# Kernel tuning notes

Hardware: AMD Instinct MI355X
Metric: run time of the kernel (lower is better)

## Reference

```python
import jax, jax.numpy as jnp
import numpy as np

N = 100000
E = 1600000
D_IN, D_EMB, D_OUT = 16, 128, 2


def _mlp(x, W1, b1, W2, b2):
    return jax.nn.relu(x @ W1 + b1) @ W2 + b2


def _gcn(x, edge_index, edge_weight, W, b):
    # PyG GCNConv: x' = W x, symmetric norm with self-loops (weight 1), scatter-add, + bias
    n = x.shape[0]
    x = x @ W
    row, col = edge_index[0], edge_index[1]
    deg = jax.ops.segment_sum(edge_weight, col, num_segments=n) + 1.0  # +1 for self-loop
    dis = jax.lax.rsqrt(deg)
    norm = dis[row] * edge_weight * dis[col]                      # [E]
    agg = jax.ops.segment_sum(norm[:, None] * x[row], col, num_segments=n)
    agg = agg + (dis * dis)[:, None] * x                          # self-loop contribution
    return agg + b


def setup_inputs() -> dict:
    key = jax.random.key(0)
    ks = jax.random.split(key, 16)
    s_in = 1.0 / np.sqrt(D_IN)
    s_emb = 1.0 / np.sqrt(D_EMB)
    return {
        "x": jax.random.normal(ks[0], (N, D_IN), dtype=jnp.float32),
        "edge_index": jax.random.randint(ks[1], (2, E), 0, N, dtype=jnp.int64),
        "edge_weight": jax.random.uniform(ks[2], (E,), dtype=jnp.float32),
        # encoder MLP
        "enc_W1": jax.random.normal(ks[3], (D_IN, D_EMB), dtype=jnp.float32) * s_in,
        "enc_b1": jnp.zeros((D_EMB,), jnp.float32),
        "enc_W2": jax.random.normal(ks[4], (D_EMB, D_EMB), dtype=jnp.float32) * s_emb,
        "enc_b2": jnp.zeros((D_EMB,), jnp.float32),
        # conv1 / conv2
        "c1_W": jax.random.normal(ks[5], (D_EMB, D_EMB), dtype=jnp.float32) * s_emb,
        "c1_b": jnp.zeros((D_EMB,), jnp.float32),
        "c2_W": jax.random.normal(ks[6], (D_EMB, D_EMB), dtype=jnp.float32) * s_emb,
        "c2_b": jnp.zeros((D_EMB,), jnp.float32),
        # decoder MLP
        "dec_W1": jax.random.normal(ks[7], (D_EMB, D_EMB), dtype=jnp.float32) * s_emb,
        "dec_b1": jnp.zeros((D_EMB,), jnp.float32),
        "dec_W2": jax.random.normal(ks[8], (D_EMB, D_OUT), dtype=jnp.float32) * s_emb,
        "dec_b2": jnp.zeros((D_OUT,), jnp.float32),
    }


def reference(x, edge_index, edge_weight,
              enc_W1, enc_b1, enc_W2, enc_b2,
              c1_W, c1_b, c2_W, c2_b,
              dec_W1, dec_b1, dec_W2, dec_b2):
    h = _mlp(x, enc_W1, enc_b1, enc_W2, enc_b2)
    h = jax.nn.relu(_gcn(h, edge_index, edge_weight, c1_W, c1_b))
    h = jax.nn.relu(_gcn(h, edge_index, edge_weight, c2_W, c2_b))
    h = _mlp(h, dec_W1, dec_b1, dec_W2, dec_b2)
    return jax.nn.softmax(h, axis=1)
```

## Files before the change

kernel.cpp:

```cpp
#include <hip/hip_runtime.h>

#define N_NODES 100000
#define N_EDGES 1600000
#define NBKT 391
#define BKT_CAP 4608
#define PART_BLOCKS 782

typedef _Float16 half8 __attribute__((ext_vector_type(8)));
typedef float floatx4 __attribute__((ext_vector_type(4)));


__global__ __launch_bounds__(256) void k_part(const int* __restrict__ ei,
                                              const float* __restrict__ ew,
                                              unsigned* __restrict__ cursor,
                                              unsigned* __restrict__ partA,
                                              float* __restrict__ partB) {
    __shared__ unsigned hist[NBKT];
    __shared__ unsigned lrank[NBKT];
    __shared__ unsigned basebuf[NBKT];
    int tid = threadIdx.x;
    int e0 = blockIdx.x * 2048 + tid * 8;
    for (int i = tid; i < NBKT; i += 256) { hist[i] = 0; lrank[i] = 0; }
    __syncthreads();

    unsigned bk[8];
    bool full = (e0 + 8 <= N_EDGES);
    if (full) {
        #pragma unroll
        for (int v = 0; v < 2; v++) {
            int4 c = *(const int4*)(ei + N_EDGES + e0 + v * 4);
            bk[v * 4 + 0] = (unsigned)c.x >> 8;
            bk[v * 4 + 1] = (unsigned)c.y >> 8;
            bk[v * 4 + 2] = (unsigned)c.z >> 8;
            bk[v * 4 + 3] = (unsigned)c.w >> 8;
        }
        #pragma unroll
        for (int i = 0; i < 8; i++) atomicAdd(&hist[bk[i]], 1u);
    } else {
        for (int i = 0; i < 8; i++) {
            if (e0 + i < N_EDGES) {
                bk[i] = (unsigned)ei[N_EDGES + e0 + i] >> 8;
                atomicAdd(&hist[bk[i]], 1u);
            }
        }
    }
    __syncthreads();
    for (int b = tid; b < NBKT; b += 256) {
        unsigned h = hist[b];
        basebuf[b] = h ? atomicAdd(&cursor[b], h) : 0u;
    }
    __syncthreads();

    if (full) {
        #pragma unroll
        for (int v = 0; v < 2; v++) {
            int4 c = *(const int4*)(ei + N_EDGES + e0 + v * 4);
            int4 r = *(const int4*)(ei + e0 + v * 4);
            float4 w = *(const float4*)(ew + e0 + v * 4);
            int cols[4] = {c.x, c.y, c.z, c.w};
            int rows[4] = {r.x, r.y, r.z, r.w};
            float ws4[4] = {w.x, w.y, w.z, w.w};
            #pragma unroll
            for (int i = 0; i < 4; i++) {
                unsigned b = bk[v * 4 + i];
                unsigned rk = atomicAdd(&lrank[b], 1u);
                size_t idx = (size_t)b * BKT_CAP + basebuf[b] + rk;
                partA[idx] = (((unsigned)cols[i] & 255u) << 17) | (unsigned)rows[i];
                partB[idx] = ws4[i];
            }
        }
    } else {
        for (int i = 0; i < 8; i++) {
            if (e0 + i < N_EDGES) {
                int col = ei[N_EDGES + e0 + i];
                int row = ei[e0 + i];
                float wv = ew[e0 + i];
                unsigned b = bk[i];
                unsigned rk = atomicAdd(&lrank[b], 1u);
                size_t idx = (size_t)b * BKT_CAP + basebuf[b] + rk;
                partA[idx] = (((unsigned)col & 255u) << 17) | (unsigned)row;
                partB[idx] = wv;
            }
        }
    }
}

__global__ __launch_bounds__(256) void k_stats(const unsigned* __restrict__ cursor,
                                               const unsigned* __restrict__ partA,
                                               const float* __restrict__ partB,
                                               float* __restrict__ dis,
                                               int* __restrict__ offs,
                                               int* __restrict__ cnt) {
    __shared__ unsigned hist[256];
    __shared__ unsigned sc[256];
    __shared__ float dacc[256];
    int tid = threadIdx.x;
    int j = blockIdx.x;
    int count = (int)cursor[j];
    size_t p0 = (size_t)j * BKT_CAP;
    hist[tid] = 0;
    dacc[tid] = 0.f;
    __syncthreads();
    for (int i = tid; i < count; i += 256) {
        unsigned a = partA[p0 + i];
        float w = partB[p0 + i];
        unsigned cl = (a >> 17) & 255u;
        atomicAdd(&hist[cl], 1u);
        atomicAdd(&dacc[cl], w);
    }
    __syncthreads();
    unsigned myc = hist[tid];
    sc[tid] = myc;
    __syncthreads();
    #pragma unroll
    for (int d = 1; d < 256; d <<= 1) {
        unsigned t = (tid >= d) ? sc[tid - d] : 0u;
        __syncthreads();
        sc[tid] += t;
        __syncthreads();
    }
    int col = j * 256 + tid;
    if (col < N_NODES) {
        dis[col] = rsqrtf(dacc[tid] + 1.0f);
        cnt[col] = (int)myc;
        offs[col] = (int)(p0 + (sc[tid] - myc));
    }
}

__global__ __launch_bounds__(256) void k_scatter(const unsigned* __restrict__ cursor,
                                                 const unsigned* __restrict__ partA,
                                                 const float* __restrict__ partB,
                                                 const int* __restrict__ offs,
                                                 const float* __restrict__ dis,
                                                 unsigned* __restrict__ csr,
                                                 float* __restrict__ svec) {
    __shared__ unsigned cur[256];
    __shared__ float sacc[256];
    int tid = threadIdx.x;
    int j = blockIdx.x;
    int count = (int)cursor[j];
    size_t p0 = (size_t)j * BKT_CAP;
    int col = j * 256 + tid;
    cur[tid] = (col < N_NODES) ? (unsigned)(offs[col] - (int)p0) : 0u;
    sacc[tid] = 0.f;
    __syncthreads();
    for (int i = tid; i < count; i += 256) {
        unsigned a = partA[p0 + i];
        float wv = partB[p0 + i];
        unsigned cl = (a >> 17) & 255u;
        unsigned row = a & 0x1FFFFu;
        unsigned r = atomicAdd(&cur[cl], 1u);
        int colg = j * 256 + (int)cl;
        float w = dis[row] * wv * dis[colg];
        _Float16 hw = (_Float16)w;
        unsigned short hb;
        __builtin_memcpy(&hb, &hw, 2);
        csr[p0 + r] = ((unsigned)hb << 17) | row;
        atomicAdd(&sacc[cl], (float)hw);
    }
    __syncthreads();
    if (col < N_NODES) {
        float d = dis[col];
        svec[col] = sacc[tid] + d * d;
    }
}

__global__ __launch_bounds__(256) void prep_mm(const float* __restrict__ W2,
                                               const float* __restrict__ c1W,
                                               _Float16* __restrict__ Wt0) {
    __shared__ float sW[128 * 128];
    int t = threadIdx.x;
    for (int i = t; i < 4096; i += 256) ((float4*)sW)[i] = ((const float4*)c1W)[i];
    __syncthreads();
    int k = blockIdx.x * 2 + (t >> 7);
    int col = t & 127;
    float acc = 0.f;
    #pragma unroll 8
    for (int j = 0; j < 128; j++) acc = fmaf(W2[k * 128 + j], sW[j * 128 + col], acc);
    Wt0[col * 128 + k] = (_Float16)acc;
}

__global__ __launch_bounds__(128) void prep_bb(const float* __restrict__ b2,
                                               const float* __restrict__ c1W,
                                               float* __restrict__ bb) {
    int c = threadIdx.x;
    float acc = 0.f;
    for (int j = 0; j < 128; j++) acc = fmaf(b2[j], c1W[j * 128 + c], acc);
    bb[c] = acc;
}

__global__ __launch_bounds__(256) void prep_tr(const float* __restrict__ Wa,
                                               const float* __restrict__ Wb,
                                               _Float16* __restrict__ Wt) {
    int m = blockIdx.x >> 4;
    const float* W = (m == 0) ? Wa : Wb;
    _Float16* o = Wt + (m + 1) * 16384;
    int base = (blockIdx.x & 15) * 1024 + threadIdx.x * 4;
    int col = base >> 7;
    int k0 = base & 127;
    #pragma unroll
    for (int i = 0; i < 4; i++) o[base + i] = (_Float16)W[(k0 + i) * 128 + col];
}


__global__ __launch_bounds__(256) void enc1_kernel(const float* __restrict__ x,
                                                   const float* __restrict__ W1,
                                                   const float* __restrict__ b1,
                                                   _Float16* __restrict__ out) {
    __shared__ float sX[256 * 17];
    __shared__ float sW[2048];
    __shared__ float sb[128];
    int t = threadIdx.x;
    int base = blockIdx.x * 256;
    for (int i = t; i < 512; i += 256) ((float4*)sW)[i] = ((const float4*)W1)[i];
    if (t < 128) sb[t] = b1[t];
    #pragma unroll
    for (int i = 0; i < 4; i++) {
        int f = i * 1024 + t * 4;
        int row = f >> 4, k = f & 15;
        float4 v = make_float4(0.f, 0.f, 0.f, 0.f);
        if (base + row < N_NODES) v = *(const float4*)(x + (size_t)(base + row) * 16 + k);
        *(float4*)(sX + row * 17 + k) = v;
    }
    __syncthreads();
    int row = base + t;
    if (row >= N_NODES) return;
    float xr[16];
    #pragma unroll
    for (int k = 0; k < 16; k++) xr[k] = sX[t * 17 + k];
    #pragma unroll 4
    for (int cb = 0; cb < 16; cb++) {
        float acc[8];
        #pragma unroll
        for (int jj = 0; jj < 8; jj++) acc[jj] = sb[cb * 8 + jj];
        #pragma unroll
        for (int k = 0; k < 16; k++) {
            float xv = xr[k];
            #pragma unroll
            for (int jj = 0; jj < 8; jj++) acc[jj] = fmaf(xv, sW[k * 128 + cb * 8 + jj], acc[jj]);
        }
        half8 h;
        #pragma unroll
        for (int jj = 0; jj < 8; jj++) h[jj] = (_Float16)fmaxf(acc[jj], 0.f);
        *(half8*)(out + (size_t)row * 128 + cb * 8) = h;
    }
}


template <bool BIAS, bool RELU, bool DEC, bool SB>
__global__ __launch_bounds__(256, 2) void gemm_mfma(const _Float16* __restrict__ A,
                                                    const _Float16* __restrict__ Wt,
                                                    const float* __restrict__ bias,
                                                    _Float16* __restrict__ C,
                                                    const float* __restrict__ W2,
                                                    const float* __restrict__ b2,
                                                    float* __restrict__ sm_out,
                                                    const float* __restrict__ svec,
                                                    const float* __restrict__ bbv) {
    __shared__ _Float16 sA[2 * 64 * 128];
    __shared__ _Float16 sE[DEC ? 64 : 64 * 128];
    __shared__ float sW2[DEC ? 256 : 1];
    int t = threadIdx.x;
    int lane = t & 63;
    int w = t >> 6;
    int l15 = lane & 15;
    int l4 = lane >> 4;
    int stride = gridDim.x;

    half8 bfrag[8][4];
    #pragma unroll
    for (int n = 0; n < 8; n++)
        #pragma unroll
        for (int kk = 0; kk < 4; kk++)
            bfrag[n][kk] = *(const half8*)(Wt + (n * 16 + l15) * 128 + kk * 32 + l4 * 8);

    float bcol[8];
    if constexpr (BIAS) {
        #pragma unroll
        for (int n = 0; n < 8; n++) bcol[n] = bias[n * 16 + l15];
    }
    float bbcol[8];
    if constexpr (SB) {
        #pragma unroll
        for (int n = 0; n < 8; n++) bbcol[n] = bbv[n * 16 + l15];
    }
    float b20 = 0.f, b21 = 0.f;
    if constexpr (DEC) {
        if (t < 256) sW2[t] = W2[t];
        b20 = b2[0]; b21 = b2[1];
    }

    auto STAGE = [&](int buf, int tile) {
        const _Float16* Ag = A + (size_t)tile * 64 * 128;
        #pragma unroll
        for (int i = 0; i < 4; i++) {
            int c = i * 256 + t;
            int row = c >> 4;
            int g = (c & 15) ^ (row & 7);
            const _Float16* src = Ag + row * 128 + g * 8;
            __builtin_amdgcn_global_load_lds(
                (const __attribute__((address_space(1))) void*)src,
                (__attribute__((address_space(3))) void*)(sA + buf * 8192 + (size_t)(i * 256 + w * 64) * 8),
                16, 0, 0);
        }
    };

    const int NT = (N_NODES + 63) / 64;
    int cur = 0;
    STAGE(0, blockIdx.x);

    for (int tile = blockIdx.x; tile < NT; tile += stride) {
        int nx = tile + stride;
        if (nx < NT) {
            STAGE(cur ^ 1, nx);
            asm volatile("s_waitcnt vmcnt(4)" ::: "memory");
        } else {
            asm volatile("s_waitcnt vmcnt(0)" ::: "memory");
        }
        __builtin_amdgcn_s_barrier();
        asm volatile("" ::: "memory");

        const _Float16* sAc = sA + cur * 8192;

        floatx4 acc[8];
        #pragma unroll
        for (int n = 0; n < 8; n++) acc[n] = (floatx4)(0.f);

        #pragma unroll
        for (int kk = 0; kk < 4; kk++) {
            int rloc = w * 16 + l15;
            int cl = kk * 4 + l4;
            int s = cl ^ (rloc & 7);
            half8 af = *(const half8*)(sAc + rloc * 128 + s * 8);
            #pragma unroll
            for (int n = 0; n < 8; n++)
                acc[n] = __builtin_amdgcn_mfma_f32_16x16x32_f16(af, bfrag[n][kk], acc[n], 0, 0, 0);
        }

        size_t base_row = (size_t)tile * 64;
        float s4[4];
        if constexpr (SB) {
            #pragma unroll
            for (int r = 0; r < 4; r++) {
                int rr = (int)base_row + w * 16 + l4 * 4 + r;
                s4[r] = (rr < N_NODES) ? svec[rr] : 0.f;
            }
        }
        if constexpr (DEC) {
            #pragma unroll
            for (int r = 0; r < 4; r++) {
                float p0 = 0.f, p1 = 0.f;
                #pragma unroll
                for (int n = 0; n < 8; n++) {
                    float v = acc[n][r];
                    if constexpr (BIAS) v += bcol[n];
                    if constexpr (RELU) v = fmaxf(v, 0.f);
                    int ch = n * 16 + l15;
                    p0 = fmaf(v, sW2[ch * 2 + 0], p0);
                    p1 = fmaf(v, sW2[ch * 2 + 1], p1);
                }
                #pragma unroll
                for (int m = 1; m < 16; m <<= 1) {
                    p0 += __shfl_xor(p0, m, 64);
                    p1 += __shfl_xor(p1, m, 64);
                }
                size_t grow = base_row + w * 16 + l4 * 4 + r;
                if (l15 == 0 && grow < N_NODES) {
                    float z0 = p0 + b20, z1 = p1 + b21;
                    float mx = fmaxf(z0, z1);
                    float e0 = expf(z0 - mx), e1 = expf(z1 - mx);
                    float si = 1.f / (e0 + e1);
                    *(float2*)(sm_out + grow * 2) = make_float2(e0 * si, e1 * si);
                }
            }
            __builtin_amdgcn_s_barrier();
            asm volatile("" ::: "memory");
        } else {
            #pragma unroll
            for (int n = 0; n < 8; n++) {
                #pragma unroll
                for (int r = 0; r < 4; r++) {
                    float v = acc[n][r];
                    if constexpr (SB) v += s4[r] * bbcol[n];
                    if constexpr (BIAS) v += bcol[n];
                    if constexpr (RELU) v = fmaxf(v, 0.f);
                    int row = w * 16 + l4 * 4 + r;
                    sE[row * 128 + n * 16 + l15] = (_Float16)v;
                }
            }
            __builtin_amdgcn_s_barrier();
            asm volatile("" ::: "memory");
            #pragma unroll
            for (int i = 0; i < 4; i++) {
                int c = i * 256 + t;
                int row = c >> 4;
                if (base_row + row < N_NODES) {
                    *(float4*)((char*)C + (base_row + row) * 256 + (c & 15) * 16) =
                        *(const float4*)((const char*)sE + (size_t)c * 16);
                }
            }
        }
        cur ^= 1;
    }
}


__device__ __forceinline__ float wdec(unsigned u) {
    unsigned short b = (unsigned short)(u >> 17);
    _Float16 h;
    __builtin_memcpy(&h, &b, 2);
    return (float)h;
}

__global__ __launch_bounds__(256) void agg_kernel(const _Float16* __restrict__ m,
                                                  const int* __restrict__ offs,
                                                  const int* __restrict__ cnt,
                                                  const unsigned* __restrict__ csr,
                                                  const float* __restrict__ dis,
                                                  _Float16* __restrict__ out) {
    int wave = threadIdx.x >> 6;
    int lane = threadIdx.x & 63;
    int g = lane >> 4;
    int q = lane & 15;
    int j = blockIdx.x * 4 + wave;
    if (j >= N_NODES) return;
    int s = offs[j];
    int num = cnt[j];
    unsigned qoff = (unsigned)(q * 8);

    float acc[8];
    if (g == 0) {
        float d = dis[j];
        float dd = d * d;
        half8 mv = *(const half8*)(m + (((unsigned)j << 7) | qoff));
        #pragma unroll
        for (int i = 0; i < 8; i++) acc[i] = dd * (float)mv[i];
    } else {
        #pragma unroll
        for (int i = 0; i < 8; i++) acc[i] = 0.f;
    }

    for (int e = 0; e < num; e += 16) {
        float wv[4];
        unsigned off[4];
        #pragma unroll
        for (int k = 0; k < 4; k++) {
            int idx = e + k * 4 + g;
            int idc = (idx < num) ? idx : (num - 1);
            unsigned uu = csr[s + idc];
            wv[k] = (idx < num) ? wdec(uu) : 0.f;
            off[k] = ((uu & 0x1FFFFu) << 7) | qoff;
        }
        half8 r0 = *(const half8*)(m + off[0]);
        half8 r1 = *(const half8*)(m + off[1]);
        half8 r2 = *(const half8*)(m + off[2]);
        half8 r3 = *(const half8*)(m + off[3]);
        #pragma unroll
        for (int i = 0; i < 8; i++) acc[i] = fmaf(wv[0], (float)r0[i], acc[i]);
        #pragma unroll
        for (int i = 0; i < 8; i++) acc[i] = fmaf(wv[1], (float)r1[i], acc[i]);
        #pragma unroll
        for (int i = 0; i < 8; i++) acc[i] = fmaf(wv[2], (float)r2[i], acc[i]);
        #pragma unroll
        for (int i = 0; i < 8; i++) acc[i] = fmaf(wv[3], (float)r3[i], acc[i]);
    }

    #pragma unroll
    for (int i = 0; i < 8; i++) {
        acc[i] += __shfl_xor(acc[i], 16, 64);
        acc[i] += __shfl_xor(acc[i], 32, 64);
    }

    if (g == 0) {
        half8 o;
        #pragma unroll
        for (int i = 0; i < 8; i++) o[i] = (_Float16)acc[i];
        *(half8*)(out + (((unsigned)j << 7) | qoff)) = o;
    }
}


extern "C" void kernel_launch(void* const* d_in, const int* in_sizes, int n_in,
                              void* d_out, int out_size, void* d_ws, size_t ws_size,
                              hipStream_t stream) {
    const float* x      = (const float*)d_in[0];
    const int*   ei     = (const int*)d_in[1];
    const float* ew     = (const float*)d_in[2];
    const float* enc_W1 = (const float*)d_in[3];
    const float* enc_b1 = (const float*)d_in[4];
    const float* enc_W2 = (const float*)d_in[5];
    const float* enc_b2 = (const float*)d_in[6];
    const float* c1_W   = (const float*)d_in[7];
    const float* c1_b   = (const float*)d_in[8];
    const float* c2_W   = (const float*)d_in[9];
    const float* c2_b   = (const float*)d_in[10];
    const float* dec_W1 = (const float*)d_in[11];
    const float* dec_b1 = (const float*)d_in[12];
    const float* dec_W2 = (const float*)d_in[13];
    const float* dec_b2 = (const float*)d_in[14];
    float* out = (float*)d_out;

    char* ws = (char*)d_ws;
    unsigned* partA = (unsigned*)(ws);
    float*    partB = (float*)(ws + 7206912);
    _Float16* B1 = (_Float16*)(ws);
    _Float16* B2 = (_Float16*)(ws + 25600000);
    _Float16* Wt = (_Float16*)(ws + 51200000);
    unsigned* cursor = (unsigned*)(ws + 51331072);
    float* dis     = (float*)(ws + 51333120);
    int*   offs    = (int*)  (ws + 51733120);
    int*   cnt     = (int*)  (ws + 52133120);
    unsigned* csr  = (unsigned*)(ws + 52533120);
    float* svec    = (float*)(ws + 59740032);
    float* bb      = (float*)(ws + 60140032);

    hipMemsetAsync(cursor, 0, 2048, stream);

    k_part<<<PART_BLOCKS, 256, 0, stream>>>(ei, ew, cursor, partA, partB);
    k_stats<<<NBKT, 256, 0, stream>>>(cursor, partA, partB, dis, offs, cnt);
    k_scatter<<<NBKT, 256, 0, stream>>>(cursor, partA, partB, offs, dis, csr, svec);

    prep_mm<<<64, 256, 0, stream>>>(enc_W2, c1_W, Wt);
    prep_bb<<<1, 128, 0, stream>>>(enc_b2, c1_W, bb);
    prep_tr<<<32, 256, 0, stream>>>(c2_W, dec_W1, Wt);
    enc1_kernel<<<(N_NODES + 255) / 256, 256, 0, stream>>>(x, enc_W1, enc_b1, B1);

    agg_kernel<<<N_NODES / 4, 256, 0, stream>>>(B1, offs, cnt, csr, dis, B2);
    gemm_mfma<true, true, false, true><<<781, 256, 0, stream>>>(
        B2, Wt + 0 * 16384, c1_b, B1, nullptr, nullptr, nullptr, svec, bb);
    agg_kernel<<<N_NODES / 4, 256, 0, stream>>>(B1, offs, cnt, csr, dis, B2);
    gemm_mfma<true, true, false, false><<<781, 256, 0, stream>>>(
        B2, Wt + 1 * 16384, c2_b, B1, nullptr, nullptr, nullptr, nullptr, nullptr);
    gemm_mfma<true, true, true, false><<<1563, 256, 0, stream>>>(
        B1, Wt + 2 * 16384, dec_b1, nullptr, dec_W2, dec_b2, out, nullptr, nullptr);
}
```

Measured before the change: 392.2 us.

## Replace atomic edge bucketing with deterministic count/scan/place CSR build

Rebuilds the CSR preprocessing as a multi-kernel pipeline: per-chunk bucket histograms, a per-bucket prefix scan for bases, wave-ballot ranking to place packed 64-bit edge records, a per-bucket LDS sort by column, and a per-node final pass computing normalized fp16 weights. This removes global atomics and the memset, and makes edge order deterministic. The cost is more launches and serial per-thread loops in the degree and final passes. The GEMM kernels also switch to a fixed persistent grid of 522 blocks and add LDS waitcnts before barriers.

```diff
diff --git a/kernel.cpp b/kernel.cpp
--- a/kernel.cpp
+++ b/kernel.cpp
@@ -4,166 +4,214 @@
 #define N_EDGES 1600000
 #define NBKT 391
 #define BKT_CAP 4608
-#define PART_BLOCKS 782
+#define NCHUNK 782
+#define CHUNK_E 2048
+#define GEMM_GRID 522
 
 typedef _Float16 half8 __attribute__((ext_vector_type(8)));
 typedef float floatx4 __attribute__((ext_vector_type(4)));
 
 
-__global__ __launch_bounds__(256) void k_part(const int* __restrict__ ei,
-                                              const float* __restrict__ ew,
-                                              unsigned* __restrict__ cursor,
-                                              unsigned* __restrict__ partA,
-                                              float* __restrict__ partB) {
+__global__ __launch_bounds__(256) void k_count(const int* __restrict__ ei,
+                                               unsigned* __restrict__ Mcnt) {
     __shared__ unsigned hist[NBKT];
-    __shared__ unsigned lrank[NBKT];
-    __shared__ unsigned basebuf[NBKT];
     int tid = threadIdx.x;
-    int e0 = blockIdx.x * 2048 + tid * 8;
-    for (int i = tid; i < NBKT; i += 256) { hist[i] = 0; lrank[i] = 0; }
-    __syncthreads();
-
-    unsigned bk[8];
-    bool full = (e0 + 8 <= N_EDGES);
-    if (full) {
+    int e0 = blockIdx.x * CHUNK_E + tid * 8;
+    for (int i = tid; i < NBKT; i += 256) hist[i] = 0;
+    __syncthreads();
+    if (e0 + 8 <= N_EDGES) {
         #pragma unroll
         for (int v = 0; v < 2; v++) {
             int4 c = *(const int4*)(ei + N_EDGES + e0 + v * 4);
-            bk[v * 4 + 0] = (unsigned)c.x >> 8;
-            bk[v * 4 + 1] = (unsigned)c.y >> 8;
-            bk[v * 4 + 2] = (unsigned)c.z >> 8;
-            bk[v * 4 + 3] = (unsigned)c.w >> 8;
-        }
-        #pragma unroll
-        for (int i = 0; i < 8; i++) atomicAdd(&hist[bk[i]], 1u);
+            atomicAdd(&hist[(unsigned)c.x >> 8], 1u);
+            atomicAdd(&hist[(unsigned)c.y >> 8], 1u);
+            atomicAdd(&hist[(unsigned)c.z >> 8], 1u);
+            atomicAdd(&hist[(unsigned)c.w >> 8], 1u);
+        }
     } else {
         for (int i = 0; i < 8; i++) {
-            if (e0 + i < N_EDGES) {
-                bk[i] = (unsigned)ei[N_EDGES + e0 + i] >> 8;
-                atomicAdd(&hist[bk[i]], 1u);
-            }
-        }
-    }
-    __syncthreads();
-    for (int b = tid; b < NBKT; b += 256) {
-        unsigned h = hist[b];
-        basebuf[b] = h ? atomicAdd(&cursor[b], h) : 0u;
-    }
-    __syncthreads();
-
-    if (full) {
-        #pragma unroll
-        for (int v = 0; v < 2; v++) {
-            int4 c = *(const int4*)(ei + N_EDGES + e0 + v * 4);
-            int4 r = *(const int4*)(ei + e0 + v * 4);
-            float4 w = *(const float4*)(ew + e0 + v * 4);
-            int cols[4] = {c.x, c.y, c.z, c.w};
-            int rows[4] = {r.x, r.y, r.z, r.w};
-            float ws4[4] = {w.x, w.y, w.z, w.w};
-            #pragma unroll
-            for (int i = 0; i < 4; i++) {
-                unsigned b = bk[v * 4 + i];
-                unsigned rk = atomicAdd(&lrank[b], 1u);
-                size_t idx = (size_t)b * BKT_CAP + basebuf[b] + rk;
-                partA[idx] = (((unsigned)cols[i] & 255u) << 17) | (unsigned)rows[i];
-                partB[idx] = ws4[i];
-            }
-        }
-    } else {
-        for (int i = 0; i < 8; i++) {
-            if (e0 + i < N_EDGES) {
-                int col = ei[N_EDGES + e0 + i];
-                int row = ei[e0 + i];
-                float wv = ew[e0 + i];
-                unsigned b = bk[i];
-                unsigned rk = atomicAdd(&lrank[b], 1u);
-                size_t idx = (size_t)b * BKT_CAP + basebuf[b] + rk;
-                partA[idx] = (((unsigned)col & 255u) << 17) | (unsigned)row;
-                partB[idx] = wv;
-            }
-        }
-    }
-}
-
-__global__ __launch_bounds__(256) void k_stats(const unsigned* __restrict__ cursor,
-                                               const unsigned* __restrict__ partA,
-                                               const float* __restrict__ partB,
-                                               float* __restrict__ dis,
-                                               int* __restrict__ offs,
-                                               int* __restrict__ cnt) {
+            if (e0 + i < N_EDGES)
+                atomicAdd(&hist[(unsigned)ei[N_EDGES + e0 + i] >> 8], 1u);
+        }
+    }
+    __syncthreads();
+    for (int i = tid; i < NBKT; i += 256) Mcnt[i * NCHUNK + blockIdx.x] = hist[i];
+}
+
+__global__ __launch_bounds__(256) void k_base(const unsigned* __restrict__ Mcnt,
+                                              unsigned* __restrict__ Mbase,
+                                              unsigned* __restrict__ btot) {
+    __shared__ unsigned s[256];
+    int t = threadIdx.x;
+    int j = blockIdx.x;
+    const unsigned* src = Mcnt + (size_t)j * NCHUNK;
+    unsigned* dst = Mbase + (size_t)j * NCHUNK;
+    unsigned carry = 0;
+    for (int seg = 0; seg < NCHUNK; seg += 256) {
+        int idx = seg + t;
+        unsigned v = (idx < NCHUNK) ? src[idx] : 0u;
+        s[t] = v;
+        __syncthreads();
+        for (int d = 1; d < 256; d <<= 1) {
+            unsigned u = (t >= d) ? s[t - d] : 0u;
+            __syncthreads();
+            s[t] += u;
+            __syncthreads();
+        }
+        if (idx < NCHUNK) dst[idx] = s[t] - v + carry;
+        carry += s[255];
+        __syncthreads();
+    }
+    if (t == 0) btot[j] = carry;
+}
+
+
+__global__ __launch_bounds__(64) void k_place(const int* __restrict__ ei,
+                                              const float* __restrict__ ew,
+                                              const unsigned* __restrict__ Mbase,
+                                              unsigned long long* __restrict__ part) {
+    __shared__ unsigned lrank[NBKT];
+    int lane = threadIdx.x;
+    int p = blockIdx.x;
+    int e0 = p * CHUNK_E;
+    int nloc = N_EDGES - e0; if (nloc > CHUNK_E) nloc = CHUNK_E;
+    for (int i = lane; i < NBKT; i += 64) lrank[i] = Mbase[i * NCHUNK + p];
+    __syncthreads();
+    for (int it = 0; it < CHUNK_E; it += 64) {
+        if (it >= nloc) break;
+        int li = it + lane;
+        bool valid = li < nloc;
+        unsigned col = 0, row = 0; float wv = 0.f;
+        if (valid) {
+            col = (unsigned)ei[N_EDGES + e0 + li];
+            row = (unsigned)ei[e0 + li];
+            wv = ew[e0 + li];
+        }
+        unsigned bk = col >> 8;
+        unsigned long long m = __ballot(valid ? 1 : 0);
+        #pragma unroll
+        for (int b = 0; b < 9; b++) {
+            unsigned long long bal = __ballot((bk >> b) & 1u);
+            m &= ((bk >> b) & 1u) ? bal : ~bal;
+        }
+        unsigned rank = (unsigned)__popcll(m & ((1ull << lane) - 1ull));
+        unsigned cntk = (unsigned)__popcll(m);
+        unsigned base = lrank[bk];
+        if (valid) {
+            unsigned u; __builtin_memcpy(&u, &wv, 4);
+            unsigned long long pay = ((unsigned long long)u << 32)
+                                   | (((unsigned long long)(col & 255u)) << 17)
+                                   | (unsigned long long)row;
+            part[(size_t)bk * BKT_CAP + base + rank] = pay;
+        }
+        bool leader = valid && (lane == (__ffsll((long long)m) - 1));
+        if (leader) lrank[bk] = base + cntk;
+        __syncthreads();
+    }
+}
+
+__global__ __launch_bounds__(64) void k_colsort(const unsigned* __restrict__ btot,
+                                                const unsigned long long* __restrict__ part,
+                                                unsigned long long* __restrict__ sorted,
+                                                float* __restrict__ dis,
+                                                int* __restrict__ offs,
+                                                int* __restrict__ cnt) {
+    __shared__ unsigned long long sh[BKT_CAP];
     __shared__ unsigned hist[256];
-    __shared__ unsigned sc[256];
-    __shared__ float dacc[256];
-    int tid = threadIdx.x;
+    __shared__ unsigned cbase[256];
+    __shared__ unsigned cur[256];
+    int lane = threadIdx.x;
     int j = blockIdx.x;
-    int count = (int)cursor[j];
+    int count = (int)btot[j];
     size_t p0 = (size_t)j * BKT_CAP;
-    hist[tid] = 0;
-    dacc[tid] = 0.f;
-    __syncthreads();
-    for (int i = tid; i < count; i += 256) {
-        unsigned a = partA[p0 + i];
-        float w = partB[p0 + i];
-        unsigned cl = (a >> 17) & 255u;
+    for (int i = lane; i < 256; i += 64) hist[i] = 0;
+    __syncthreads();
+    for (int i = lane; i < count; i += 64) {
+        unsigned cl = (unsigned)(part[p0 + i] >> 17) & 255u;
         atomicAdd(&hist[cl], 1u);
-        atomicAdd(&dacc[cl], w);
-    }
-    __syncthreads();
-    unsigned myc = hist[tid];
-    sc[tid] = myc;
-    __syncthreads();
-    #pragma unroll
-    for (int d = 1; d < 256; d <<= 1) {
-        unsigned t = (tid >= d) ? sc[tid - d] : 0u;
+    }
+    __syncthreads();
+    unsigned h0 = hist[lane * 4], h1 = hist[lane * 4 + 1];
+    unsigned h2 = hist[lane * 4 + 2], h3 = hist[lane * 4 + 3];
+    unsigned lsum = h0 + h1 + h2 + h3;
+    unsigned inc = lsum;
+    #pragma unroll
+    for (int d = 1; d < 64; d <<= 1) {
+        unsigned u = __shfl_up(inc, d, 64);
+        if (lane >= d) inc += u;
+    }
+    unsigned lex = inc - lsum;
+    cbase[lane * 4]     = lex;
+    cbase[lane * 4 + 1] = lex + h0;
+    cbase[lane * 4 + 2] = lex + h0 + h1;
+    cbase[lane * 4 + 3] = lex + h0 + h1 + h2;
+    __syncthreads();
+    for (int i = lane; i < 256; i += 64) cur[i] = cbase[i];
+    __syncthreads();
+    for (int it = 0; it < count; it += 64) {
+        int i = it + lane;
+        bool valid = i < count;
+        unsigned long long v = valid ? part[p0 + i] : 0ull;
+        unsigned cl = (unsigned)(v >> 17) & 255u;
+        unsigned long long m = __ballot(valid ? 1 : 0);
+        #pragma unroll
+        for (int b = 0; b < 8; b++) {
+            unsigned long long bal = __ballot((cl >> b) & 1u);
+            m &= ((cl >> b) & 1u) ? bal : ~bal;
+        }
+        unsigned rank = (unsigned)__popcll(m & ((1ull << lane) - 1ull));
+        unsigned base = cur[cl];
+        if (valid) sh[base + rank] = v;
+        bool leader = valid && (lane == (__ffsll((long long)m) - 1));
+        if (leader) cur[cl] = base + (unsigned)__popcll(m);
         __syncthreads();
-        sc[tid] += t;
-        __syncthreads();
-    }
-    int col = j * 256 + tid;
-    if (col < N_NODES) {
-        dis[col] = rsqrtf(dacc[tid] + 1.0f);
-        cnt[col] = (int)myc;
-        offs[col] = (int)(p0 + (sc[tid] - myc));
-    }
-}
-
-__global__ __launch_bounds__(256) void k_scatter(const unsigned* __restrict__ cursor,
-                                                 const unsigned* __restrict__ partA,
-                                                 const float* __restrict__ partB,
-                                                 const int* __restrict__ offs,
-                                                 const float* __restrict__ dis,
-                                                 unsigned* __restrict__ csr,
-                                                 float* __restrict__ svec) {
-    __shared__ unsigned cur[256];
-    __shared__ float sacc[256];
-    int tid = threadIdx.x;
-    int j = blockIdx.x;
-    int count = (int)cursor[j];
-    size_t p0 = (size_t)j * BKT_CAP;
-    int col = j * 256 + tid;
-    cur[tid] = (col < N_NODES) ? (unsigned)(offs[col] - (int)p0) : 0u;
-    sacc[tid] = 0.f;
-    __syncthreads();
-    for (int i = tid; i < count; i += 256) {
-        unsigned a = partA[p0 + i];
-        float wv = partB[p0 + i];
-        unsigned cl = (a >> 17) & 255u;
-        unsigned row = a & 0x1FFFFu;
-        unsigned r = atomicAdd(&cur[cl], 1u);
-        int colg = j * 256 + (int)cl;
-        float w = dis[row] * wv * dis[colg];
+    }
+    for (int i = lane; i < count; i += 64) sorted[p0 + i] = sh[i];
+    #pragma unroll
+    for (int k = 0; k < 4; k++) {
+        int c = lane * 4 + k;
+        int col = j * 256 + c;
+        if (col >= N_NODES) continue;
+        unsigned n = hist[c];
+        unsigned b = cbase[c];
+        float deg = 0.f;
+        for (unsigned i = 0; i < n; i++) {
+            unsigned u = (unsigned)(sh[b + i] >> 32);
+            float wv; __builtin_memcpy(&wv, &u, 4);
+            deg += wv;
+        }
+        dis[col] = rsqrtf(deg + 1.0f);
+        cnt[col] = (int)n;
+        offs[col] = (int)(p0 + b);
+    }
+}
+
+__global__ __launch_bounds__(256) void k_final(const unsigned long long* __restrict__ sorted,
+                                               const float* __restrict__ dis,
+                                               const int* __restrict__ offs,
+                                               const int* __restrict__ cnt,
+                                               unsigned* __restrict__ csr,
+                                               float* __restrict__ svec) {
+    int col = blockIdx.x * 256 + threadIdx.x;
+    if (col >= N_NODES) return;
+    int n = cnt[col];
+    int o = offs[col];
+    float dc = dis[col];
+    float ssum = 0.f;
+    for (int i = 0; i < n; i++) {
+        unsigned long long v = sorted[(size_t)o + i];
+        unsigned u = (unsigned)(v >> 32);
+        float wv; __builtin_memcpy(&wv, &u, 4);
+        unsigned row = (unsigned)(v & 0x1FFFFu);
+        float w = dis[row] * wv * dc;
         _Float16 hw = (_Float16)w;
-        unsigned short hb;
-        __builtin_memcpy(&hb, &hw, 2);
-        csr[p0 + r] = ((unsigned)hb << 17) | row;
-        atomicAdd(&sacc[cl], (float)hw);
-    }
-    __syncthreads();
-    if (col < N_NODES) {
-        float d = dis[col];
-        svec[col] = sacc[tid] + d * d;
-    }
-}
+        unsigned short hb; __builtin_memcpy(&hb, &hw, 2);
+        csr[(size_t)o + i] = ((unsigned)hb << 17) | row;
+        ssum += (float)hw;
+    }
+    svec[col] = ssum + dc * dc;
+}
+
 
 __global__ __launch_bounds__(256) void prep_mm(const float* __restrict__ W2,
                                                const float* __restrict__ c1W,
@@ -265,7 +313,6 @@
     int w = t >> 6;
     int l15 = lane & 15;
     int l4 = lane >> 4;
-    int stride = gridDim.x;
 
     half8 bfrag[8][4];
     #pragma unroll
@@ -309,13 +356,13 @@
     int cur = 0;
     STAGE(0, blockIdx.x);
 
-    for (int tile = blockIdx.x; tile < NT; tile += stride) {
-        int nx = tile + stride;
+    for (int tile = blockIdx.x; tile < NT; tile += GEMM_GRID) {
+        int nx = tile + GEMM_GRID;
         if (nx < NT) {
             STAGE(cur ^ 1, nx);
-            asm volatile("s_waitcnt vmcnt(4)" ::: "memory");
+            asm volatile("s_waitcnt vmcnt(4) lgkmcnt(0)" ::: "memory");
         } else {
-            asm volatile("s_waitcnt vmcnt(0)" ::: "memory");
+            asm volatile("s_waitcnt vmcnt(0) lgkmcnt(0)" ::: "memory");
         }
         __builtin_amdgcn_s_barrier();
         asm volatile("" ::: "memory");
@@ -373,6 +420,7 @@
                     *(float2*)(sm_out + grow * 2) = make_float2(e0 * si, e1 * si);
                 }
             }
+            asm volatile("s_waitcnt lgkmcnt(0)" ::: "memory");
             __builtin_amdgcn_s_barrier();
             asm volatile("" ::: "memory");
         } else {
@@ -388,6 +436,7 @@
                     sE[row * 128 + n * 16 + l15] = (_Float16)v;
                 }
             }
+            asm volatile("s_waitcnt lgkmcnt(0)" ::: "memory");
             __builtin_amdgcn_s_barrier();
             asm volatile("" ::: "memory");
             #pragma unroll
@@ -501,24 +550,26 @@
     float* out = (float*)d_out;
 
     char* ws = (char*)d_ws;
-    unsigned* partA = (unsigned*)(ws);
-    float*    partB = (float*)(ws + 7206912);
+    unsigned long long* part   = (unsigned long long*)(ws);
+    unsigned* Mcnt  = (unsigned*)(ws + 14413824);
+    unsigned* Mbase = (unsigned*)(ws + 15636872);
+    unsigned* btot  = (unsigned*)(ws + 16859920);
+    unsigned long long* sorted = (unsigned long long*)(ws + 16861488);
     _Float16* B1 = (_Float16*)(ws);
     _Float16* B2 = (_Float16*)(ws + 25600000);
     _Float16* Wt = (_Float16*)(ws + 51200000);
-    unsigned* cursor = (unsigned*)(ws + 51331072);
-    float* dis     = (float*)(ws + 51333120);
-    int*   offs    = (int*)  (ws + 51733120);
-    int*   cnt     = (int*)  (ws + 52133120);
-    unsigned* csr  = (unsigned*)(ws + 52533120);
-    float* svec    = (float*)(ws + 59740032);
-    float* bb      = (float*)(ws + 60140032);
-
-    hipMemsetAsync(cursor, 0, 2048, stream);
-
-    k_part<<<PART_BLOCKS, 256, 0, stream>>>(ei, ew, cursor, partA, partB);
-    k_stats<<<NBKT, 256, 0, stream>>>(cursor, partA, partB, dis, offs, cnt);
-    k_scatter<<<NBKT, 256, 0, stream>>>(cursor, partA, partB, offs, dis, csr, svec);
+    float* dis  = (float*)(ws + 51331072);
+    int*   offs = (int*)  (ws + 51731072);
+    int*   cnt  = (int*)  (ws + 52131072);
+    unsigned* csr = (unsigned*)(ws + 52531072);
+    float* svec = (float*)(ws + 59737984);
+    float* bb   = (float*)(ws + 60137984);
+
+    k_count<<<NCHUNK, 256, 0, stream>>>(ei, Mcnt);
+    k_base<<<NBKT, 256, 0, stream>>>(Mcnt, Mbase, btot);
+    k_place<<<NCHUNK, 64, 0, stream>>>(ei, ew, Mbase, part);
+    k_colsort<<<NBKT, 64, 0, stream>>>(btot, part, sorted, dis, offs, cnt);
+    k_final<<<NBKT, 256, 0, stream>>>(sorted, dis, offs, cnt, csr, svec);
 
     prep_mm<<<64, 256, 0, stream>>>(enc_W2, c1_W, Wt);
     prep_bb<<<1, 128, 0, stream>>>(enc_b2, c1_W, bb);
@@ -526,11 +577,11 @@
     enc1_kernel<<<(N_NODES + 255) / 256, 256, 0, stream>>>(x, enc_W1, enc_b1, B1);
 
     agg_kernel<<<N_NODES / 4, 256, 0, stream>>>(B1, offs, cnt, csr, dis, B2);
-    gemm_mfma<true, true, false, true><<<781, 256, 0, stream>>>(
+    gemm_mfma<true, true, false, true><<<GEMM_GRID, 256, 0, stream>>>(
         B2, Wt + 0 * 16384, c1_b, B1, nullptr, nullptr, nullptr, svec, bb);
     agg_kernel<<<N_NODES / 4, 256, 0, stream>>>(B1, offs, cnt, csr, dis, B2);
-    gemm_mfma<true, true, false, false><<<781, 256, 0, stream>>>(
+    gemm_mfma<true, true, false, false><<<GEMM_GRID, 256, 0, stream>>>(
         B2, Wt + 1 * 16384, c2_b, B1, nullptr, nullptr, nullptr, nullptr, nullptr);
-    gemm_mfma<true, true, true, false><<<1563, 256, 0, stream>>>(
+    gemm_mfma<true, true, true, false><<<GEMM_GRID, 256, 0, stream>>>(
         B1, Wt + 2 * 16384, dec_b1, nullptr, dec_W2, dec_b2, out, nullptr, nullptr);
 }
```

New measurement: 437.7 us. 1.12x slower.
